# Kernel tuning notes

Measured on AMD Instinct MI355X. Metric: run time of the kernel, lower is better.

## Reference

```python
import jax, jax.numpy as jnp
import numpy as np

B, S, DIM = 4, 4096, 1024
H, HD = 16, 64  # n_heads, head_dim = dim // n_heads
UMV = 20.0      # unified_max_value (init kwarg)


def setup_inputs() -> dict:
    key = jax.random.key(0)
    kx, kw = jax.random.split(key)
    x = jax.random.normal(kx, (B, S, DIM), dtype=jnp.float32)
    # qkv_proj: Linear(dim, 3*dim). Small weight scale + positive bias keeps
    # attention scores inside the keep-window [0, 2*UMV] so denominators are safe.
    W_qkv = jax.random.normal(kw, (DIM, 3 * DIM), dtype=jnp.float32) * 0.02
    b_qkv = jnp.full((3 * DIM,), 0.5, dtype=jnp.float32)
    return {"x": x, "W_qkv": W_qkv, "b_qkv": b_qkv}


def reference(x, W_qkv, b_qkv):
    Bb, Ss, _ = x.shape
    qkv = x @ W_qkv + b_qkv                      # [B,S,3*dim]
    qkv = qkv.reshape(Bb, Ss, H, 3 * HD)          # [B,S,H,3*hd]
    Q, K, V = jnp.split(qkv, 3, axis=-1)          # each [B,S,H,hd]
    # matmul(Q, K.transpose(-2,-1)) on [B,S,H,hd]: contract head_dim -> [B,S,H,H]
    s = jnp.einsum('bshd,bsgd->bshg', Q, K) - UMV
    e = jnp.exp(s)
    mask = (s > UMV) | (s < -UMV)                 # keep only s in [-UMV, UMV]
    e = jnp.where(mask, 0.0, e)
    denom = jnp.sum(e, axis=-1, keepdims=True)
    p = e / denom                                  # [B,S,H,H]
    out = jnp.einsum('bshg,bsgd->bshd', p, V)      # [B,S,H,hd]
    return out
```

## Files before the change

kernel.cpp:

```cpp
#include <hip/hip_runtime.h>

typedef _Float16 v8h __attribute__((ext_vector_type(8)));
typedef _Float16 v4h __attribute__((ext_vector_type(4)));
typedef _Float16 v2h __attribute__((ext_vector_type(2)));
typedef float v4f __attribute__((ext_vector_type(4)));

__device__ __forceinline__ void gl16(const void* g, void* l) {
    __builtin_amdgcn_global_load_lds(
        (const __attribute__((address_space(1))) unsigned int*)g,
        (__attribute__((address_space(3))) unsigned int*)l, 16, 0, 0);
}

__device__ __forceinline__ void wave_lds_fence() {
    asm volatile("s_waitcnt lgkmcnt(0)" ::: "memory");
}

__global__ __launch_bounds__(256) void k_cvt(const float* __restrict__ x,
                                             _Float16* __restrict__ x16,
                                             const float* __restrict__ W,
                                             _Float16* __restrict__ Wt) {
    if (blockIdx.x < 8192) {
        int i = (blockIdx.x * 256 + threadIdx.x) * 8;
        float4 a = *(const float4*)(x + i);
        float4 b = *(const float4*)(x + i + 4);
        v8h h;
        h[0] = (_Float16)a.x; h[1] = (_Float16)a.y; h[2] = (_Float16)a.z; h[3] = (_Float16)a.w;
        h[4] = (_Float16)b.x; h[5] = (_Float16)b.y; h[6] = (_Float16)b.z; h[7] = (_Float16)b.w;
        *(v8h*)(x16 + i) = h;
    } else {
        __shared__ float T[64][68];
        int bid = blockIdx.x - 8192;
        int k0 = (bid & 15) * 64;
        int n0 = (bid >> 4) * 64;
        int t = threadIdx.x;
        int tr = t >> 4;
        int tc = t & 15;
#pragma unroll
        for (int rr = 0; rr < 4; rr++) {
            int kk = rr * 16 + tr;
            float4 v = *(const float4*)(W + (size_t)(k0 + kk) * 3072 + n0 + tc * 4);
            T[kk][tc * 4 + 0] = v.x; T[kk][tc * 4 + 1] = v.y;
            T[kk][tc * 4 + 2] = v.z; T[kk][tc * 4 + 3] = v.w;
        }
        __syncthreads();
#pragma unroll
        for (int ww = 0; ww < 4; ww++) {
            int nn = ww * 16 + tr;
            v4h h;
#pragma unroll
            for (int i = 0; i < 4; i++) h[i] = (_Float16)T[tc * 4 + i][nn];
            *(v4h*)(Wt + (size_t)(n0 + nn) * 1024 + k0 + tc * 4) = h;
        }
    }
}

__global__ __launch_bounds__(256) void k_gemm(const _Float16* __restrict__ A,
                                              const _Float16* __restrict__ Bt,
                                              const float* __restrict__ bias,
                                              _Float16* __restrict__ C) {
    __shared__ __align__(16) _Float16 As[128 * 32];
    __shared__ __align__(16) _Float16 Bs[128 * 32];
    int bm = blockIdx.x & 127;
    int bn = blockIdx.x >> 7;
    int m0 = bm * 128, n0 = bn * 128;
    int tid = threadIdx.x;
    int w = tid >> 6, lane = tid & 63;
    int quad = lane >> 4, l15 = lane & 15;
    int wm = (w & 1) * 64, wn = (w >> 1) * 64;

    int mc1 = w * 16 + (lane >> 2);
    int mc2 = (w + 4) * 16 + (lane >> 2);
    int k8 = (lane & 3) * 8;
    const _Float16* aS1 = A + (size_t)(m0 + mc1) * 1024 + k8;
    const _Float16* aS2 = A + (size_t)(m0 + mc2) * 1024 + k8;
    const _Float16* bS1 = Bt + (size_t)(n0 + mc1) * 1024 + k8;
    const _Float16* bS2 = Bt + (size_t)(n0 + mc2) * 1024 + k8;
    _Float16* lA1 = &As[w * 512];
    _Float16* lA2 = &As[(w + 4) * 512];
    _Float16* lB1 = &Bs[w * 512];
    _Float16* lB2 = &Bs[(w + 4) * 512];

    v4f acc[4][4] = {};

    for (int kt = 0; kt < 1024; kt += 32) {
        __syncthreads();
        gl16(aS1 + kt, lA1);
        gl16(aS2 + kt, lA2);
        gl16(bS1 + kt, lB1);
        gl16(bS2 + kt, lB2);
        __syncthreads();
        v8h af[4], bf[4];
#pragma unroll
        for (int mi = 0; mi < 4; mi++)
            af[mi] = *(const v8h*)&As[(wm + mi * 16 + l15) * 32 + quad * 8];
#pragma unroll
        for (int ni = 0; ni < 4; ni++)
            bf[ni] = *(const v8h*)&Bs[(wn + ni * 16 + l15) * 32 + quad * 8];
#pragma unroll
        for (int mi = 0; mi < 4; mi++)
#pragma unroll
            for (int ni = 0; ni < 4; ni++)
                acc[mi][ni] = __builtin_amdgcn_mfma_f32_16x16x32_f16(af[mi], bf[ni], acc[mi][ni], 0, 0, 0);
    }

#pragma unroll
    for (int ni = 0; ni < 4; ni++) {
        int n = n0 + wn + ni * 16 + l15;
        float bv = bias[n];
#pragma unroll
        for (int mi = 0; mi < 4; mi++) {
            int mbase = m0 + wm + mi * 16 + quad * 4;
#pragma unroll
            for (int r = 0; r < 4; r++)
                C[(size_t)(mbase + r) * 3072 + n] = (_Float16)(acc[mi][ni][r] + bv);
        }
    }
}

__global__ __launch_bounds__(256) void k_attn(const _Float16* __restrict__ qkv,
                                              float* __restrict__ out) {
    __shared__ __align__(16) _Float16 Lh[4][16 * 200];
    __shared__ float Pb[4][16 * 17];
    int tid = threadIdx.x;
    int w = tid >> 6, lane = tid & 63;
    int pos = blockIdx.x * 4 + w;
    _Float16* L = Lh[w];
    float* P = Pb[w];
    const _Float16* src = qkv + (size_t)pos * 3072;

#pragma unroll
    for (int ii = 0; ii < 6; ii++) {
        int e = (ii * 64 + lane) * 8;
        v8h v = *(const v8h*)(src + e);
        int h = e / 192, r = e % 192;
        *(v8h*)(L + h * 200 + r) = v;
    }
    wave_lds_fence();

    int l15 = lane & 15, quad = lane >> 4;
    {
        const _Float16* row = L + l15 * 200;
        v8h a0 = *(const v8h*)(row + quad * 8);
        v8h a1 = *(const v8h*)(row + 32 + quad * 8);
        v8h b0 = *(const v8h*)(row + 64 + quad * 8);
        v8h b1 = *(const v8h*)(row + 96 + quad * 8);
        v4f s = {};
        s = __builtin_amdgcn_mfma_f32_16x16x32_f16(a0, b0, s, 0, 0, 0);
        s = __builtin_amdgcn_mfma_f32_16x16x32_f16(a1, b1, s, 0, 0, 0);
        float e4[4];
#pragma unroll
        for (int r = 0; r < 4; r++) {
            float sv = s[r] - 20.0f;
            e4[r] = (sv > 20.0f || sv < -20.0f) ? 0.0f : __expf(sv);
        }
#pragma unroll
        for (int r = 0; r < 4; r++) {
            float t = e4[r];
            t += __shfl_xor(t, 1, 64);
            t += __shfl_xor(t, 2, 64);
            t += __shfl_xor(t, 4, 64);
            t += __shfl_xor(t, 8, 64);
            P[(quad * 4 + r) * 17 + l15] = e4[r] / t;
        }
    }
    wave_lds_fence();

    {
        int h2 = lane >> 2, db = (lane & 3) * 16;
        v2h o2[8] = {};
#pragma unroll
        for (int g = 0; g < 16; g++) {
            _Float16 ph = (_Float16)P[h2 * 17 + g];
            v2h p2; p2[0] = ph; p2[1] = ph;
            const _Float16* Vr = L + g * 200 + 128 + db;
            v8h v0 = *(const v8h*)(Vr);
            v8h v1 = *(const v8h*)(Vr + 8);
#pragma unroll
            for (int j = 0; j < 4; j++) {
                o2[j]     = p2 * ((v2h*)&v0)[j] + o2[j];
                o2[4 + j] = p2 * ((v2h*)&v1)[j] + o2[4 + j];
            }
        }
        float* dst = out + (size_t)pos * 1024 + h2 * 64 + db;
#pragma unroll
        for (int d4 = 0; d4 < 4; d4++) {
            float4 v;
            v.x = (float)o2[d4 * 2][0];
            v.y = (float)o2[d4 * 2][1];
            v.z = (float)o2[d4 * 2 + 1][0];
            v.w = (float)o2[d4 * 2 + 1][1];
            *(float4*)(dst + d4 * 4) = v;
        }
    }
}

extern "C" void kernel_launch(void* const* d_in, const int* in_sizes, int n_in,
                              void* d_out, int out_size, void* d_ws, size_t ws_size,
                              hipStream_t stream) {
    (void)in_sizes; (void)n_in; (void)out_size; (void)ws_size;
    const float* x  = (const float*)d_in[0];
    const float* Wq = (const float*)d_in[1];
    const float* bq = (const float*)d_in[2];
    float* out = (float*)d_out;

    char* ob = (char*)d_out;
    _Float16* x16   = (_Float16*)ob;
    _Float16* wt16  = (_Float16*)(ob + (48u << 20));
    _Float16* qkv16 = (_Float16*)d_ws;

    k_cvt<<<8960, 256, 0, stream>>>(x, x16, Wq, wt16);
    k_gemm<<<3072, 256, 0, stream>>>(x16, wt16, bq, qkv16);
    k_attn<<<4096, 256, 0, stream>>>(qkv16, out);
}
```

Measured before the change: 289.9 us.

## Widen GEMM K-tile with XOR-swizzled LDS and restructure attention PV stage

The GEMM now stages a 64-wide K tile per iteration, halving the number of barrier pairs, and XOR-swizzles the 16-byte chunks in LDS so the fragment reads avoid bank conflicts. The attention kernel stores probabilities as fp16 in padded rows and has each lane compute 4 output elements across four heads. This gives coalesced, contiguous float4 stores and fewer redundant V reads. The larger LDS footprint (32 KB per GEMM block) may reduce occupancy, and the fp16 probabilities are rounded earlier than before.

```diff
diff --git a/kernel.cpp b/kernel.cpp
--- a/kernel.cpp
+++ b/kernel.cpp
@@ -58,8 +58,8 @@
                                               const _Float16* __restrict__ Bt,
                                               const float* __restrict__ bias,
                                               _Float16* __restrict__ C) {
-    __shared__ __align__(16) _Float16 As[128 * 32];
-    __shared__ __align__(16) _Float16 Bs[128 * 32];
+    __shared__ __align__(16) _Float16 As[128 * 64];
+    __shared__ __align__(16) _Float16 Bs[128 * 64];
     int bm = blockIdx.x & 127;
     int bn = blockIdx.x >> 7;
     int m0 = bm * 128, n0 = bn * 128;
@@ -68,39 +68,49 @@
     int quad = lane >> 4, l15 = lane & 15;
     int wm = (w & 1) * 64, wn = (w >> 1) * 64;
 
-    int mc1 = w * 16 + (lane >> 2);
-    int mc2 = (w + 4) * 16 + (lane >> 2);
-    int k8 = (lane & 3) * 8;
-    const _Float16* aS1 = A + (size_t)(m0 + mc1) * 1024 + k8;
-    const _Float16* aS2 = A + (size_t)(m0 + mc2) * 1024 + k8;
-    const _Float16* bS1 = Bt + (size_t)(n0 + mc1) * 1024 + k8;
-    const _Float16* bS2 = Bt + (size_t)(n0 + mc2) * 1024 + k8;
-    _Float16* lA1 = &As[w * 512];
-    _Float16* lA2 = &As[(w + 4) * 512];
-    _Float16* lB1 = &Bs[w * 512];
-    _Float16* lB2 = &Bs[(w + 4) * 512];
+    const _Float16* aG[4];
+    const _Float16* bG[4];
+    _Float16 *lA[4], *lB[4];
+#pragma unroll
+    for (int j = 0; j < 4; j++) {
+        int s = w * 256 + j * 64 + lane;
+        int row = s >> 3, c = s & 7;
+        int gc = c ^ (row & 7);
+        aG[j] = A  + (size_t)(m0 + row) * 1024 + gc * 8;
+        bG[j] = Bt + (size_t)(n0 + row) * 1024 + gc * 8;
+        lA[j] = &As[s * 8];
+        lB[j] = &Bs[s * 8];
+    }
 
     v4f acc[4][4] = {};
 
-    for (int kt = 0; kt < 1024; kt += 32) {
+    for (int it = 0; it < 16; it++) {
         __syncthreads();
-        gl16(aS1 + kt, lA1);
-        gl16(aS2 + kt, lA2);
-        gl16(bS1 + kt, lB1);
-        gl16(bS2 + kt, lB2);
+        int kt = it * 64;
+#pragma unroll
+        for (int j = 0; j < 4; j++) gl16(aG[j] + kt, lA[j]);
+#pragma unroll
+        for (int j = 0; j < 4; j++) gl16(bG[j] + kt, lB[j]);
         __syncthreads();
-        v8h af[4], bf[4];
-#pragma unroll
-        for (int mi = 0; mi < 4; mi++)
-            af[mi] = *(const v8h*)&As[(wm + mi * 16 + l15) * 32 + quad * 8];
-#pragma unroll
-        for (int ni = 0; ni < 4; ni++)
-            bf[ni] = *(const v8h*)&Bs[(wn + ni * 16 + l15) * 32 + quad * 8];
-#pragma unroll
-        for (int mi = 0; mi < 4; mi++)
-#pragma unroll
-            for (int ni = 0; ni < 4; ni++)
-                acc[mi][ni] = __builtin_amdgcn_mfma_f32_16x16x32_f16(af[mi], bf[ni], acc[mi][ni], 0, 0, 0);
+#pragma unroll
+        for (int ks = 0; ks < 2; ks++) {
+            v8h af[4], bf[4];
+#pragma unroll
+            for (int mi = 0; mi < 4; mi++) {
+                int row = wm + mi * 16 + l15;
+                af[mi] = *(const v8h*)&As[row * 64 + (((ks << 2) | quad) ^ (row & 7)) * 8];
+            }
+#pragma unroll
+            for (int ni = 0; ni < 4; ni++) {
+                int row = wn + ni * 16 + l15;
+                bf[ni] = *(const v8h*)&Bs[row * 64 + (((ks << 2) | quad) ^ (row & 7)) * 8];
+            }
+#pragma unroll
+            for (int mi = 0; mi < 4; mi++)
+#pragma unroll
+                for (int ni = 0; ni < 4; ni++)
+                    acc[mi][ni] = __builtin_amdgcn_mfma_f32_16x16x32_f16(af[mi], bf[ni], acc[mi][ni], 0, 0, 0);
+        }
     }
 
 #pragma unroll
@@ -120,12 +130,12 @@
 __global__ __launch_bounds__(256) void k_attn(const _Float16* __restrict__ qkv,
                                               float* __restrict__ out) {
     __shared__ __align__(16) _Float16 Lh[4][16 * 200];
-    __shared__ float Pb[4][16 * 17];
+    __shared__ __align__(16) _Float16 Pb[4][16 * 24];
     int tid = threadIdx.x;
     int w = tid >> 6, lane = tid & 63;
     int pos = blockIdx.x * 4 + w;
     _Float16* L = Lh[w];
-    float* P = Pb[w];
+    _Float16* P = Pb[w];
     const _Float16* src = qkv + (size_t)pos * 3072;
 
 #pragma unroll
@@ -160,36 +170,43 @@
             t += __shfl_xor(t, 2, 64);
             t += __shfl_xor(t, 4, 64);
             t += __shfl_xor(t, 8, 64);
-            P[(quad * 4 + r) * 17 + l15] = e4[r] / t;
+            P[(quad * 4 + r) * 24 + l15] = (_Float16)(e4[r] / t);
         }
     }
     wave_lds_fence();
 
     {
-        int h2 = lane >> 2, db = (lane & 3) * 16;
-        v2h o2[8] = {};
+        int q4 = lane >> 4, dl = lane & 15;
+        v8h p0[4], p1[4];
+#pragma unroll
+        for (int t = 0; t < 4; t++) {
+            const _Float16* Pr = P + (4 * t + q4) * 24;
+            p0[t] = *(const v8h*)Pr;
+            p1[t] = *(const v8h*)(Pr + 8);
+        }
+        v2h o[4][2] = {};
 #pragma unroll
         for (int g = 0; g < 16; g++) {
-            _Float16 ph = (_Float16)P[h2 * 17 + g];
-            v2h p2; p2[0] = ph; p2[1] = ph;
-            const _Float16* Vr = L + g * 200 + 128 + db;
-            v8h v0 = *(const v8h*)(Vr);
-            v8h v1 = *(const v8h*)(Vr + 8);
-#pragma unroll
-            for (int j = 0; j < 4; j++) {
-                o2[j]     = p2 * ((v2h*)&v0)[j] + o2[j];
-                o2[4 + j] = p2 * ((v2h*)&v1)[j] + o2[4 + j];
+            v4h vv = *(const v4h*)(L + g * 200 + 128 + dl * 4);
+            v2h va; va[0] = vv[0]; va[1] = vv[1];
+            v2h vb; vb[0] = vv[2]; vb[1] = vv[3];
+#pragma unroll
+            for (int t = 0; t < 4; t++) {
+                _Float16 ph = (g < 8) ? p0[t][g] : p1[t][g - 8];
+                v2h p2; p2[0] = ph; p2[1] = ph;
+                o[t][0] = p2 * va + o[t][0];
+                o[t][1] = p2 * vb + o[t][1];
             }
         }
-        float* dst = out + (size_t)pos * 1024 + h2 * 64 + db;
-#pragma unroll
-        for (int d4 = 0; d4 < 4; d4++) {
+        float* dst = out + (size_t)pos * 1024;
+#pragma unroll
+        for (int t = 0; t < 4; t++) {
             float4 v;
-            v.x = (float)o2[d4 * 2][0];
-            v.y = (float)o2[d4 * 2][1];
-            v.z = (float)o2[d4 * 2 + 1][0];
-            v.w = (float)o2[d4 * 2 + 1][1];
-            *(float4*)(dst + d4 * 4) = v;
+            v.x = (float)o[t][0][0];
+            v.y = (float)o[t][0][1];
+            v.z = (float)o[t][1][0];
+            v.w = (float)o[t][1][1];
+            *(float4*)(dst + t * 256 + lane * 4) = v;
         }
     }
 }
```

Measured after the change: 275.4 us. 5.0% less time.

## Load Q/K/V directly from global into registers in attention kernel, skip LDS staging

Applied to the files above, without the earlier changes.

The attention kernel no longer copies each position's QKV row into shared memory. The MFMA operands for Q and K are loaded straight from global memory, and each lane keeps a 4-element V segment per head in registers. Softmax probabilities are stored as fp16 in a smaller LDS buffer. The PV product is remapped so each lane computes 4 output heads over a contiguous 4-wide slice of head_dim, which gives fully coalesced float4 output stores. This removes the LDS round trip and its fence, at the cost of scattered global loads and more register pressure.

```diff
diff --git a/kernel.cpp b/kernel.cpp
--- a/kernel.cpp
+++ b/kernel.cpp
@@ -119,31 +119,26 @@
 
 __global__ __launch_bounds__(256) void k_attn(const _Float16* __restrict__ qkv,
                                               float* __restrict__ out) {
-    __shared__ __align__(16) _Float16 Lh[4][16 * 200];
-    __shared__ float Pb[4][16 * 17];
+    __shared__ __align__(16) _Float16 Pb[4][16 * 24];
     int tid = threadIdx.x;
     int w = tid >> 6, lane = tid & 63;
     int pos = blockIdx.x * 4 + w;
-    _Float16* L = Lh[w];
-    float* P = Pb[w];
+    _Float16* P = Pb[w];
     const _Float16* src = qkv + (size_t)pos * 3072;
-
-#pragma unroll
-    for (int ii = 0; ii < 6; ii++) {
-        int e = (ii * 64 + lane) * 8;
-        v8h v = *(const v8h*)(src + e);
-        int h = e / 192, r = e % 192;
-        *(v8h*)(L + h * 200 + r) = v;
-    }
-    wave_lds_fence();
-
     int l15 = lane & 15, quad = lane >> 4;
+
+    const _Float16* hrow = src + l15 * 192;
+    v8h a0 = *(const v8h*)(hrow + quad * 8);
+    v8h a1 = *(const v8h*)(hrow + 32 + quad * 8);
+    v8h b0 = *(const v8h*)(hrow + 64 + quad * 8);
+    v8h b1 = *(const v8h*)(hrow + 96 + quad * 8);
+    int dl = lane & 15;
+    v4h vseg[16];
+#pragma unroll
+    for (int g = 0; g < 16; g++)
+        vseg[g] = *(const v4h*)(src + g * 192 + 128 + dl * 4);
+
     {
-        const _Float16* row = L + l15 * 200;
-        v8h a0 = *(const v8h*)(row + quad * 8);
-        v8h a1 = *(const v8h*)(row + 32 + quad * 8);
-        v8h b0 = *(const v8h*)(row + 64 + quad * 8);
-        v8h b1 = *(const v8h*)(row + 96 + quad * 8);
         v4f s = {};
         s = __builtin_amdgcn_mfma_f32_16x16x32_f16(a0, b0, s, 0, 0, 0);
         s = __builtin_amdgcn_mfma_f32_16x16x32_f16(a1, b1, s, 0, 0, 0);
@@ -160,36 +155,41 @@
             t += __shfl_xor(t, 2, 64);
             t += __shfl_xor(t, 4, 64);
             t += __shfl_xor(t, 8, 64);
-            P[(quad * 4 + r) * 17 + l15] = e4[r] / t;
+            P[(quad * 4 + r) * 24 + l15] = (_Float16)(e4[r] / t);
         }
     }
     wave_lds_fence();
 
     {
-        int h2 = lane >> 2, db = (lane & 3) * 16;
-        v2h o2[8] = {};
+        v8h p0[4], p1[4];
+#pragma unroll
+        for (int t = 0; t < 4; t++) {
+            const _Float16* Pr = P + (4 * t + quad) * 24;
+            p0[t] = *(const v8h*)Pr;
+            p1[t] = *(const v8h*)(Pr + 8);
+        }
+        v2h o[4][2] = {};
 #pragma unroll
         for (int g = 0; g < 16; g++) {
-            _Float16 ph = (_Float16)P[h2 * 17 + g];
-            v2h p2; p2[0] = ph; p2[1] = ph;
-            const _Float16* Vr = L + g * 200 + 128 + db;
-            v8h v0 = *(const v8h*)(Vr);
-            v8h v1 = *(const v8h*)(Vr + 8);
-#pragma unroll
-            for (int j = 0; j < 4; j++) {
-                o2[j]     = p2 * ((v2h*)&v0)[j] + o2[j];
-                o2[4 + j] = p2 * ((v2h*)&v1)[j] + o2[4 + j];
+            v2h va; va[0] = vseg[g][0]; va[1] = vseg[g][1];
+            v2h vb; vb[0] = vseg[g][2]; vb[1] = vseg[g][3];
+#pragma unroll
+            for (int t = 0; t < 4; t++) {
+                _Float16 ph = (g < 8) ? p0[t][g] : p1[t][g - 8];
+                v2h p2; p2[0] = ph; p2[1] = ph;
+                o[t][0] = p2 * va + o[t][0];
+                o[t][1] = p2 * vb + o[t][1];
             }
         }
-        float* dst = out + (size_t)pos * 1024 + h2 * 64 + db;
-#pragma unroll
-        for (int d4 = 0; d4 < 4; d4++) {
+        float* dst = out + (size_t)pos * 1024;
+#pragma unroll
+        for (int t = 0; t < 4; t++) {
             float4 v;
-            v.x = (float)o2[d4 * 2][0];
-            v.y = (float)o2[d4 * 2][1];
-            v.z = (float)o2[d4 * 2 + 1][0];
-            v.w = (float)o2[d4 * 2 + 1][1];
-            *(float4*)(dst + d4 * 4) = v;
+            v.x = (float)o[t][0][0];
+            v.y = (float)o[t][0][1];
+            v.z = (float)o[t][1][0];
+            v.w = (float)o[t][1][1];
+            *(float4*)(dst + t * 256 + lane * 4) = v;
         }
     }
 }
```

New measurement: 272.6 us. -6.0%, faster.
